# Kernel optimization log

Hardware: AMD Instinct MI355X
Metric: run time of the kernel (lower is better)

## Reference

```python
import jax, jax.numpy as jnp
import numpy as np

GROUP_SIZE = 64  # init_kwargs: group_size
BATCH = 1024
NEURONS = 65536  # must be divisible by GROUP_SIZE


def setup_inputs() -> dict:
    key = jax.random.key(0)
    kx, kp = jax.random.split(key)
    # positive activations (firing rates) so group sums are nonzero
    x = jax.random.uniform(kx, (BATCH, NEURONS), dtype=jnp.float32)
    # build()'s np.random.shuffle(np.arange(neuron_num)) -> fixed random permutation
    index = jax.random.permutation(kp, jnp.arange(NEURONS, dtype=jnp.int32))
    return {"x": x, "index": index}


def reference(x, index):
    # x: [B, N] activations; index: [N] permutation defining group membership.
    # Group g = permuted neurons [g*GROUP_SIZE, (g+1)*GROUP_SIZE).
    B, N = x.shape
    gathered = x[:, index].reshape(B, N // GROUP_SIZE, GROUP_SIZE)  # [B, G, gs]
    norm = gathered / jnp.sum(gathered, axis=-1, keepdims=True)     # divisive normalization
    # scatter back to original neuron positions: out[:, index] = norm
    out = jnp.zeros_like(x).at[:, index].set(norm.reshape(B, N))
    return out
```

## Files before the change

### kernel.cpp

```cpp
#include <hip/hip_runtime.h>
#include <hip/hip_bf16.h>

#define BATCH   1024
#define NEUR    65536
#define NGRP    1024
#define NCHUNK  8
#define CHUNK   (NEUR / NCHUNK)
#define CHUNK_F4 (CHUNK / 4)
#define BLK1    512
#define F4T1    (CHUNK_F4 / BLK1)
#define KMAX    16
#define SENT    CHUNK
#define BLK     1024
#define ROW_F4  (NEUR / 4)
#define HALF_F4 (ROW_F4 / 2)
#define H_ITERS (HALF_F4 / BLK)
#define BUCKET_ELEMS (NCHUNK * NGRP * KMAX)
#define SPILL_CAP 1024

typedef float          f32x4 __attribute__((ext_vector_type(4)));
typedef unsigned short u16x8 __attribute__((ext_vector_type(8)));
typedef unsigned short u16x4 __attribute__((ext_vector_type(4)));


__global__ void build_tables(const int* __restrict__ index,
                             unsigned short* __restrict__ gof,
                             unsigned short* __restrict__ bucket,
                             unsigned int* __restrict__ spill) {
    const int p    = blockIdx.x * blockDim.x + threadIdx.x;
    const int lane = threadIdx.x & 63;
    const int g    = p >> 6;
    const int s    = index[p];
    gof[s] = (unsigned short)g;
    const int c = s >> 13;
    unsigned long long mc = 0;
    int count[NCHUNK];
    #pragma unroll
    for (int cc = 0; cc < NCHUNK; ++cc) {
        unsigned long long m = __ballot(c == cc);
        if (cc == c) mc = m;
        count[cc] = __popcll(m);
    }
    const int k = __popcll(mc & ((1ull << lane) - 1ull));
    if (k < KMAX) {
        bucket[((size_t)(c * NGRP + g)) * KMAX + k] = (unsigned short)(s & (CHUNK - 1));
    } else {
        unsigned int pos = atomicAdd(spill, 1u);
        if (pos < SPILL_CAP - 1)
            spill[1 + pos] = ((unsigned)g << 16) | (unsigned)s;
    }
    #pragma unroll
    for (int j = 0; j < 2; ++j) {
        const int slot = lane + j * 64;
        const int cc = slot >> 4, kk = slot & 15;
        if (kk >= count[cc])
            bucket[((size_t)(cc * NGRP + g)) * KMAX + kk] = (unsigned short)SENT;
    }
}

__global__ __launch_bounds__(BLK1, 8)
void k1_partial(const float* __restrict__ x,
                const unsigned short* __restrict__ bucket,
                const unsigned int* __restrict__ spill,
                float* __restrict__ part) {
    __shared__ float xs[CHUNK + 16];
    const int bc = blockIdx.x;
    const int b  = bc >> 3;
    const int c  = bc & 7;
    const int t  = threadIdx.x;

    const unsigned short* __restrict__ bk0 =
        bucket + ((size_t)(c * NGRP + t)) * KMAX;
    const unsigned short* __restrict__ bk1 =
        bucket + ((size_t)(c * NGRP + t + 512)) * KMAX;
    const u16x8 w0 = *(const u16x8*)(bk0);
    const u16x8 w1 = *(const u16x8*)(bk0 + 8);
    const u16x8 w2 = *(const u16x8*)(bk1);
    const u16x8 w3 = *(const u16x8*)(bk1 + 8);
    const unsigned int ns = spill[0];

    if (t == 0) xs[SENT] = 0.0f;

    const float4* __restrict__ src =
        (const float4*)(x + (size_t)b * NEUR + (size_t)c * CHUNK);
    float4* xs4 = (float4*)xs;
    #pragma unroll
    for (int i = 0; i < F4T1; ++i) {
        __builtin_amdgcn_global_load_lds(
            (const __attribute__((address_space(1))) unsigned int*)(src + i * BLK1 + t),
            (__attribute__((address_space(3))) unsigned int*)(xs4 + i * BLK1 + t),
            16, 0, 0);
    }
    __syncthreads();

    float a0 = 0.0f, a1 = 0.0f, b0 = 0.0f, b1 = 0.0f;
    #pragma unroll
    for (int j = 0; j < 8; ++j) {
        a0 += xs[w0[j]];
        a1 += xs[w1[j]];
        b0 += xs[w2[j]];
        b1 += xs[w3[j]];
    }

    for (unsigned int e = 0; e < ns; ++e) {
        const unsigned int ent = spill[1 + e];
        if (((ent >> 13) & 7u) == (unsigned)c) {
            const float v = xs[ent & 0x1FFFu];
            const int gg = (int)(ent >> 16);
            if (gg == t)            a1 += v;
            else if (gg == t + 512) b1 += v;
        }
    }

    float* __restrict__ prow = part + ((size_t)b * NCHUNK + c) * NGRP;
    prow[t]       = a0 + a1;
    prow[t + 512] = b0 + b1;
}

__global__ __launch_bounds__(BLK, 8)
void k3_scale(const float* __restrict__ x,
              const unsigned short* __restrict__ gof,
              const float* __restrict__ part,
              float* __restrict__ out) {
    __shared__ float rsum[NGRP];
    const int rb   = blockIdx.x;
    const int b    = (BATCH - 1) - (rb >> 1);
    const int half = rb & 1;
    const int t    = threadIdx.x;

    const float* __restrict__ prow = part + (size_t)b * NCHUNK * NGRP;
    float s = 0.0f;
    #pragma unroll
    for (int c = 0; c < NCHUNK; ++c) s += prow[c * NGRP + t];
    rsum[t] = 1.0f / s;
    __syncthreads();

    const float4* __restrict__ xrow4 = (const float4*)(x + (size_t)b * NEUR);
    const u16x4*  __restrict__ gof4  = (const u16x4*)gof;
    f32x4*        __restrict__ orow4 = (f32x4*)(out + (size_t)b * NEUR);

    #pragma unroll
    for (int it = 0; it < H_ITERS; ++it) {
        const int e = half * HALF_F4 + it * BLK + t;
        const float4 v = xrow4[e];
        const u16x4 g = gof4[e];
        f32x4 o;
        o.x = v.x * rsum[g.x];
        o.y = v.y * rsum[g.y];
        o.z = v.z * rsum[g.z];
        o.w = v.w * rsum[g.w];
        __builtin_nontemporal_store(o, &orow4[e]);
    }
}

extern "C" void kernel_launch(void* const* d_in, const int* in_sizes, int n_in,
                              void* d_out, int out_size, void* d_ws, size_t ws_size,
                              hipStream_t stream) {
    const float* x     = (const float*)d_in[0];
    const int*   index = (const int*)d_in[1];
    float*       out   = (float*)d_out;

    unsigned short* gof    = (unsigned short*)d_ws;
    unsigned short* bucket = gof + NEUR;
    float*          part   = (float*)(bucket + BUCKET_ELEMS);
    unsigned int*   spill  = (unsigned int*)(part + (size_t)BATCH * NCHUNK * NGRP);

    hipMemsetAsync(spill, 0, sizeof(unsigned int), stream);
    build_tables<<<NEUR / BLK, BLK, 0, stream>>>(index, gof, bucket, spill);
    k1_partial<<<BATCH * NCHUNK, BLK1, 0, stream>>>(x, bucket, spill, part);
    k3_scale<<<BATCH * 2, BLK, 0, stream>>>(x, gof, part, out);
}
```

Measured before the change: 147.2 us.

## Fuse partial-sum and scale kernels into persistent producer/consumer kernel

Replaces the separate partial-sum and scaling kernels with one persistent kernel: 512 producer blocks compute per-chunk group partial sums and signal per-row counters with release atomics, while 512 consumer blocks spin on those counters and then normalize and write rows. The aim is to overlap the second read pass with the first and to drop a kernel boundary. The cost is spin-waiting, atomics and a reliance on all 1024 blocks being co-resident, since consumers could deadlock if producers are not scheduled.

New measurement: 568.1 us. 286% more time.

```diff
diff --git a/kernel.cpp b/kernel.cpp
--- a/kernel.cpp
+++ b/kernel.cpp
@@ -7,16 +7,20 @@
 #define NCHUNK  8
 #define CHUNK   (NEUR / NCHUNK)
 #define CHUNK_F4 (CHUNK / 4)
-#define BLK1    512
-#define F4T1    (CHUNK_F4 / BLK1)
+#define BLKT    512
+#define F4T1    (CHUNK_F4 / BLKT)
 #define KMAX    16
 #define SENT    CHUNK
 #define BLK     1024
 #define ROW_F4  (NEUR / 4)
 #define HALF_F4 (ROW_F4 / 2)
-#define H_ITERS (HALF_F4 / BLK)
+#define CONS_ITERS (HALF_F4 / BLKT)
 #define BUCKET_ELEMS (NCHUNK * NGRP * KMAX)
 #define SPILL_CAP 1024
+#define NPROD   512
+#define NCONS   512
+#define A_ITEMS (BATCH * NCHUNK)
+#define B_ITEMS (BATCH * 2)
 
 typedef float          f32x4 __attribute__((ext_vector_type(4)));
 typedef unsigned short u16x8 __attribute__((ext_vector_type(8)));
@@ -58,98 +62,124 @@
     }
 }
 
-__global__ __launch_bounds__(BLK1, 8)
-void k1_partial(const float* __restrict__ x,
-                const unsigned short* __restrict__ bucket,
-                const unsigned int* __restrict__ spill,
-                float* __restrict__ part) {
+__global__ __launch_bounds__(BLKT, 8)
+void fused(const float* __restrict__ x,
+           const unsigned short* __restrict__ gof,
+           const unsigned short* __restrict__ bucket,
+           const unsigned int* __restrict__ spill,
+           float* __restrict__ part,
+           unsigned int* __restrict__ cnt,
+           float* __restrict__ out) {
     __shared__ float xs[CHUNK + 16];
-    const int bc = blockIdx.x;
-    const int b  = bc >> 3;
-    const int c  = bc & 7;
-    const int t  = threadIdx.x;
-
-    const unsigned short* __restrict__ bk0 =
-        bucket + ((size_t)(c * NGRP + t)) * KMAX;
-    const unsigned short* __restrict__ bk1 =
-        bucket + ((size_t)(c * NGRP + t + 512)) * KMAX;
-    const u16x8 w0 = *(const u16x8*)(bk0);
-    const u16x8 w1 = *(const u16x8*)(bk0 + 8);
-    const u16x8 w2 = *(const u16x8*)(bk1);
-    const u16x8 w3 = *(const u16x8*)(bk1 + 8);
-    const unsigned int ns = spill[0];
-
-    if (t == 0) xs[SENT] = 0.0f;
-
-    const float4* __restrict__ src =
-        (const float4*)(x + (size_t)b * NEUR + (size_t)c * CHUNK);
-    float4* xs4 = (float4*)xs;
-    #pragma unroll
-    for (int i = 0; i < F4T1; ++i) {
-        __builtin_amdgcn_global_load_lds(
-            (const __attribute__((address_space(1))) unsigned int*)(src + i * BLK1 + t),
-            (__attribute__((address_space(3))) unsigned int*)(xs4 + i * BLK1 + t),
-            16, 0, 0);
-    }
-    __syncthreads();
-
-    float a0 = 0.0f, a1 = 0.0f, b0 = 0.0f, b1 = 0.0f;
-    #pragma unroll
-    for (int j = 0; j < 8; ++j) {
-        a0 += xs[w0[j]];
-        a1 += xs[w1[j]];
-        b0 += xs[w2[j]];
-        b1 += xs[w3[j]];
-    }
-
-    for (unsigned int e = 0; e < ns; ++e) {
-        const unsigned int ent = spill[1 + e];
-        if (((ent >> 13) & 7u) == (unsigned)c) {
-            const float v = xs[ent & 0x1FFFu];
-            const int gg = (int)(ent >> 16);
-            if (gg == t)            a1 += v;
-            else if (gg == t + 512) b1 += v;
+    const int bid = blockIdx.x;
+    const int t   = threadIdx.x;
+
+    if (bid < NPROD) {
+        const unsigned int ns = spill[0];
+        if (t == 0) xs[SENT] = 0.0f;
+        int pending_b = -1;
+
+        for (int i = 0; i < A_ITEMS / NPROD; ++i) {
+            const int a = bid + i * NPROD;
+            const int b = a >> 3, c = a & 7;
+
+            const unsigned short* __restrict__ bk0 =
+                bucket + ((size_t)(c * NGRP + t)) * KMAX;
+            const unsigned short* __restrict__ bk1 =
+                bucket + ((size_t)(c * NGRP + t + 512)) * KMAX;
+            const u16x8 w0 = *(const u16x8*)(bk0);
+            const u16x8 w1 = *(const u16x8*)(bk0 + 8);
+            const u16x8 w2 = *(const u16x8*)(bk1);
+            const u16x8 w3 = *(const u16x8*)(bk1 + 8);
+
+            __syncthreads();
+            if (t == 0 && pending_b >= 0)
+                __hip_atomic_fetch_add(&cnt[pending_b], 1u, __ATOMIC_RELEASE,
+                                       __HIP_MEMORY_SCOPE_AGENT);
+
+            const float4* __restrict__ src =
+                (const float4*)(x + (size_t)b * NEUR + (size_t)c * CHUNK);
+            float4* xs4 = (float4*)xs;
+            #pragma unroll
+            for (int j = 0; j < F4T1; ++j) {
+                __builtin_amdgcn_global_load_lds(
+                    (const __attribute__((address_space(1))) unsigned int*)(src + j * BLKT + t),
+                    (__attribute__((address_space(3))) unsigned int*)(xs4 + j * BLKT + t),
+                    16, 0, 0);
+            }
+            __syncthreads();
+
+            float a0 = 0.0f, a1 = 0.0f, b0 = 0.0f, b1 = 0.0f;
+            #pragma unroll
+            for (int j = 0; j < 8; ++j) {
+                a0 += xs[w0[j]];
+                a1 += xs[w1[j]];
+                b0 += xs[w2[j]];
+                b1 += xs[w3[j]];
+            }
+            for (unsigned int e = 0; e < ns; ++e) {
+                const unsigned int ent = spill[1 + e];
+                if (((ent >> 13) & 7u) == (unsigned)c) {
+                    const float v = xs[ent & 0x1FFFu];
+                    const int gg = (int)(ent >> 16);
+                    if (gg == t)            a1 += v;
+                    else if (gg == t + 512) b1 += v;
+                }
+            }
+            float* __restrict__ prow = part + ((size_t)b * NCHUNK + c) * NGRP;
+            prow[t]       = a0 + a1;
+            prow[t + 512] = b0 + b1;
+            pending_b = b;
         }
-    }
-
-    float* __restrict__ prow = part + ((size_t)b * NCHUNK + c) * NGRP;
-    prow[t]       = a0 + a1;
-    prow[t + 512] = b0 + b1;
-}
-
-__global__ __launch_bounds__(BLK, 8)
-void k3_scale(const float* __restrict__ x,
-              const unsigned short* __restrict__ gof,
-              const float* __restrict__ part,
-              float* __restrict__ out) {
-    __shared__ float rsum[NGRP];
-    const int rb   = blockIdx.x;
-    const int b    = (BATCH - 1) - (rb >> 1);
-    const int half = rb & 1;
-    const int t    = threadIdx.x;
-
-    const float* __restrict__ prow = part + (size_t)b * NCHUNK * NGRP;
-    float s = 0.0f;
-    #pragma unroll
-    for (int c = 0; c < NCHUNK; ++c) s += prow[c * NGRP + t];
-    rsum[t] = 1.0f / s;
-    __syncthreads();
-
-    const float4* __restrict__ xrow4 = (const float4*)(x + (size_t)b * NEUR);
-    const u16x4*  __restrict__ gof4  = (const u16x4*)gof;
-    f32x4*        __restrict__ orow4 = (f32x4*)(out + (size_t)b * NEUR);
-
-    #pragma unroll
-    for (int it = 0; it < H_ITERS; ++it) {
-        const int e = half * HALF_F4 + it * BLK + t;
-        const float4 v = xrow4[e];
-        const u16x4 g = gof4[e];
-        f32x4 o;
-        o.x = v.x * rsum[g.x];
-        o.y = v.y * rsum[g.y];
-        o.z = v.z * rsum[g.z];
-        o.w = v.w * rsum[g.w];
-        __builtin_nontemporal_store(o, &orow4[e]);
+        __syncthreads();
+        if (t == 0 && pending_b >= 0)
+            __hip_atomic_fetch_add(&cnt[pending_b], 1u, __ATOMIC_RELEASE,
+                                   __HIP_MEMORY_SCOPE_AGENT);
+    } else {
+        float* rsum = xs;
+        const int q = bid - NPROD;
+
+        for (int i = 0; i < B_ITEMS / NCONS; ++i) {
+            const int w = q + i * NCONS;
+            const int b = w >> 1, half = w & 1;
+
+            if (t == 0) {
+                while (__hip_atomic_load(&cnt[b], __ATOMIC_ACQUIRE,
+                                         __HIP_MEMORY_SCOPE_AGENT) != NCHUNK)
+                    __builtin_amdgcn_s_sleep(8);
+            }
+            __syncthreads();
+
+            float s0 = 0.0f, s1 = 0.0f;
+            #pragma unroll
+            for (int c = 0; c < NCHUNK; ++c) {
+                const float* __restrict__ prow = part + ((size_t)b * NCHUNK + c) * NGRP;
+                s0 += __hip_atomic_load(prow + t,       __ATOMIC_RELAXED,
+                                        __HIP_MEMORY_SCOPE_AGENT);
+                s1 += __hip_atomic_load(prow + t + 512, __ATOMIC_RELAXED,
+                                        __HIP_MEMORY_SCOPE_AGENT);
+            }
+            rsum[t]       = 1.0f / s0;
+            rsum[t + 512] = 1.0f / s1;
+            __syncthreads();
+
+            const float4* __restrict__ xrow4 = (const float4*)(x + (size_t)b * NEUR);
+            const u16x4*  __restrict__ gof4  = (const u16x4*)gof;
+            f32x4*        __restrict__ orow4 = (f32x4*)(out + (size_t)b * NEUR);
+
+            #pragma unroll
+            for (int it = 0; it < CONS_ITERS; ++it) {
+                const int e = half * HALF_F4 + it * BLKT + t;
+                const float4 v = xrow4[e];
+                const u16x4 g = gof4[e];
+                f32x4 o;
+                o.x = v.x * rsum[g.x];
+                o.y = v.y * rsum[g.y];
+                o.z = v.z * rsum[g.z];
+                o.w = v.w * rsum[g.w];
+                __builtin_nontemporal_store(o, &orow4[e]);
+            }
+        }
     }
 }
 
@@ -163,10 +193,11 @@
     unsigned short* gof    = (unsigned short*)d_ws;
     unsigned short* bucket = gof + NEUR;
     float*          part   = (float*)(bucket + BUCKET_ELEMS);
-    unsigned int*   spill  = (unsigned int*)(part + (size_t)BATCH * NCHUNK * NGRP);
-
-    hipMemsetAsync(spill, 0, sizeof(unsigned int), stream);
+    unsigned int*   cnt    = (unsigned int*)(part + (size_t)BATCH * NCHUNK * NGRP);
+    unsigned int*   spill  = cnt + BATCH;
+
+    hipMemsetAsync(cnt, 0, (BATCH + 1) * sizeof(unsigned int), stream);
     build_tables<<<NEUR / BLK, BLK, 0, stream>>>(index, gof, bucket, spill);
-    k1_partial<<<BATCH * NCHUNK, BLK1, 0, stream>>>(x, bucket, spill, part);
-    k3_scale<<<BATCH * 2, BLK, 0, stream>>>(x, gof, part, out);
+    fused<<<NPROD + NCONS, BLKT, 0, stream>>>(x, gof, bucket, spill,
+                                              part, cnt, out);
 }
```
